# Kernel optimization log

Hardware: AMD Instinct MI355X
Metric: run time of the kernel (lower is better)

The kernel has to match this reference:

```python
import jax, jax.numpy as jnp
import numpy as np

MD = 4            # max_displacement
PATCH = 2 * MD + 1  # 9 displacements per axis (kernel_size=1, stride=1, pad=0)


def setup_inputs() -> dict:
    key = jax.random.key(0)
    k1, k2 = jax.random.split(key)
    feat1 = jax.random.normal(k1, (4, 256, 64, 64), jnp.float32)
    feat2 = jax.random.normal(k2, (4, 256, 64, 64), jnp.float32)
    return {"feat1": feat1, "feat2": feat2}


def _correlation(feat1, feat2, md):
    """SpatialCorrelationSampler with kernel_size=1, patch=2*md+1, stride=1, pad=0.
    out[b,di,dj,y,x] = sum_c feat1[b,c,y,x] * feat2[b,c,y+di-md, x+dj-md] (zero outside).
    Returns (B, P, P, H, W)."""
    B, C, H, W = feat1.shape
    P = 2 * md + 1
    f2p = jnp.pad(feat2, ((0, 0), (0, 0), (md, md), (md, md)))
    # fixed small loop over 81 displacements (not a data-dim loop)
    slices = [
        jnp.sum(feat1 * jax.lax.dynamic_slice(f2p, (0, 0, di, dj), (B, C, H, W)), axis=1)
        for di in range(P) for dj in range(P)
    ]
    return jnp.stack(slices, axis=1).reshape(B, P, P, H, W)


def _remap(cv, md):
    """Vectorized equivalent of remap_cost_volume's python double loop:
    out[b, r+di-md, c+dj-md, r, c] = cv[b, di, dj, r, c] for in-bounds targets."""
    B, P, _, H, W = cv.shape
    d = jnp.arange(P) - md
    r = jnp.arange(H)
    c = jnp.arange(W)
    tr = d[:, None] + r[None, :]            # (P, H) target rows
    tc = d[:, None] + c[None, :]            # (P, W) target cols
    vr = (tr >= 0) & (tr < H)
    vc = (tc >= 0) & (tc < W)
    TR = jnp.clip(tr, 0, H - 1)[:, None, :, None]   # (P,1,H,1)
    TC = jnp.clip(tc, 0, W - 1)[None, :, None, :]   # (1,P,1,W)
    mask = vr[:, None, :, None] & vc[None, :, None, :]  # (P,P,H,W)
    vals = cv * mask.astype(cv.dtype)                   # (B,P,P,H,W)
    R = r[None, None, :, None]
    Cc = c[None, None, None, :]
    TRb, TCb, Rb, Cb = jnp.broadcast_arrays(TR, TC, R, Cc)  # (P,P,H,W)
    out = jnp.zeros((B, H, W, H, W), cv.dtype)
    out = out.at[:, TRb, TCb, Rb, Cb].add(vals)
    return out


def reference(feat1, feat2):
    cv = _correlation(feat1, feat2, MD)      # (B,P,P,H,W)
    B = cv.shape[0]
    H, W = cv.shape[-2], cv.shape[-1]
    remapped = _remap(cv, MD)                # (B,H,W,H,W)
    return remapped.reshape(B, H * W, H, W)  # final .view(B,-1,rows,cols)
```

## Files before the change

### kernel.cpp

```cpp
#include <hip/hip_runtime.h>

#define MD 4
#define PATCH 9
#define NBAND 256
#define NZERO 2048
#define BT 512

__device__ __forceinline__ unsigned bf16b(float x)
{
    unsigned u = __float_as_uint(x);
    return (u + 0x7fffu + ((u >> 16) & 1u)) >> 16;
}

template<int ND>
__device__ __forceinline__ void band_core(
    const float* __restrict__ f1base,
    const unsigned (* __restrict__ sw)[72],
    int ty, int dy0, int lane,
    float acc[3][PATCH])
{
    int yoff[ND];
#pragma unroll
    for (int i = 0; i < ND; ++i) {
        int y = ty + dy0 + i - MD;
        y = y < 0 ? 0 : (y > 63 ? 63 : y);
        yoff[i] = y * 64;
    }

#pragma unroll 2
    for (int cp = 0; cp < 64; ++cp) {
        const float* c0 = f1base + (size_t)(2 * cp) * 4096;
        float f1v0[ND], f1v1[ND];
#pragma unroll
        for (int i = 0; i < ND; ++i) {
            f1v0[i] = c0[yoff[i]];
            f1v1[i] = c0[4096 + yoff[i]];
        }
        const unsigned* wp = &sw[cp][lane];
        unsigned sh2[PATCH];
#pragma unroll
        for (int dxi = 0; dxi < PATCH; ++dxi)
            sh2[dxi] = wp[8 - dxi];
#pragma unroll
        for (int dxi = 0; dxi < PATCH; ++dxi) {
            float lo = __uint_as_float(sh2[dxi] << 16);
            float hi = __uint_as_float(sh2[dxi] & 0xffff0000u);
#pragma unroll
            for (int i = 0; i < ND; ++i) {
                acc[i][dxi] = fmaf(f1v0[i], lo, acc[i][dxi]);
                acc[i][dxi] = fmaf(f1v1[i], hi, acc[i][dxi]);
            }
        }
    }
}

__global__ __launch_bounds__(BT, 8) void cv_kernel(
    const float* __restrict__ f1,
    const float* __restrict__ f2,
    float* __restrict__ out)
{
    const int tid = threadIdx.x;

    if (blockIdx.x >= NBAND) {
        float4* o4 = (float4*)out;
        const float4 z4 = make_float4(0.f, 0.f, 0.f, 0.f);
        const int total4 = 4 * 4096 * 64 * 16;
        const int stride = NZERO * BT;
        for (int i = (blockIdx.x - NBAND) * BT + tid; i < total4; i += stride) {
            int y  = (i >> 4) & 63;
            int ty = (i >> 16) & 63;
            int dy = y - ty;
            if (dy < -MD || dy > MD)
                o4[i] = z4;
        }
        return;
    }

    const int bty = blockIdx.x;
    const int b   = bty >> 6;
    const int ty  = bty & 63;
    const int lane = tid & 63;
    const int w    = tid >> 6;
    const int cq   = w >> 2;
    const int dyg  = w & 3;
    const int dy0  = dyg * 2;
    const int nd   = (dyg == 3) ? 3 : 2;

    __shared__ unsigned uLds[128 * 72];
    unsigned (*sF2)[72] = (unsigned(*)[72])uLds;

    for (int i = tid; i < 128 * 8; i += BT) {
        int c2 = i >> 3, s = i & 7;
        sF2[c2][s < 4 ? s : 64 + s] = 0u;
    }
    const float* f2b = f2 + (size_t)(b * 256) * 4096 + ty * 64;
#pragma unroll
    for (int m = 0; m < 16; ++m) {
        int e  = m * BT + tid;
        int c2 = e >> 6, x = e & 63;
        float lo = f2b[(size_t)(2 * c2) * 4096 + x];
        float hi = f2b[(size_t)(2 * c2 + 1) * 4096 + x];
        sF2[c2][4 + x] = (bf16b(hi) << 16) | bf16b(lo);
    }
    __syncthreads();

    float acc[3][PATCH];
#pragma unroll
    for (int i = 0; i < 3; ++i)
#pragma unroll
        for (int j = 0; j < PATCH; ++j) acc[i][j] = 0.f;

    const float* f1b = f1 + (size_t)(b * 256 + cq * 128) * 4096 + lane;
    const unsigned (*sw)[72] = &sF2[cq * 64];

    if (dyg == 3) band_core<3>(f1b, sw, ty, dy0, lane, acc);
    else          band_core<2>(f1b, sw, ty, dy0, lane, acc);

    __syncthreads();
    float (*sVals)[81] = (float(*)[81])uLds;

    if (cq == 0) {
#pragma unroll
        for (int i = 0; i < 3; ++i) {
            if (i >= nd) continue;
            int dyi = dy0 + i;
            int y = ty + dyi - MD;
            if ((unsigned)y >= 64u) continue;
#pragma unroll
            for (int dxi = 0; dxi < PATCH; ++dxi) {
                int tx = lane - (dxi - MD);
                if ((unsigned)tx < 64u)
                    sVals[tx][dyi * PATCH + dxi] = acc[i][dxi];
            }
        }
    }
    __syncthreads();
    if (cq != 0) {
#pragma unroll
        for (int i = 0; i < 3; ++i) {
            if (i >= nd) continue;
            int dyi = dy0 + i;
            int y = ty + dyi - MD;
            if ((unsigned)y >= 64u) continue;
#pragma unroll
            for (int dxi = 0; dxi < PATCH; ++dxi) {
                int tx = lane - (dxi - MD);
                if ((unsigned)tx < 64u)
                    atomicAdd(&sVals[tx][dyi * PATCH + dxi], acc[i][dxi]);
            }
        }
    }
    __syncthreads();

    float4* out4 = (float4*)(out + (size_t)(b * 4096 + ty * 64) * 4096);
    const int q4 = tid & 15;
    const int ro = tid >> 4;
    for (int rb = 0; rb < 64 * PATCH; rb += 32) {
        int row = rb + ro;
        int tx  = row / PATCH;
        int dyi = row - tx * PATCH;
        int y   = ty + dyi - MD;
        if ((unsigned)y < 64u) {
            float comp[4];
#pragma unroll
            for (int j = 0; j < 4; ++j) {
                int x  = q4 * 4 + j;
                int dx = x - tx;
                comp[j] = (dx >= -MD && dx <= MD) ? sVals[tx][dyi * PATCH + dx + MD] : 0.f;
            }
            out4[tx * 1024 + y * 16 + q4] = make_float4(comp[0], comp[1], comp[2], comp[3]);
        }
    }
}

extern "C" void kernel_launch(void* const* d_in, const int* in_sizes, int n_in,
                              void* d_out, int out_size, void* d_ws, size_t ws_size,
                              hipStream_t stream) {
    const float* f1 = (const float*)d_in[0];
    const float* f2 = (const float*)d_in[1];
    float* out = (float*)d_out;
    cv_kernel<<<NBAND + NZERO, BT, 0, stream>>>(f1, f2, out);
}
```

Baseline: 85.92 us.

## Double block size to split channels four ways and swizzle band block order

Each band block now has 1024 threads. The channel reduction is split into four quarters of 64 channels instead of two halves, and the number of zero-fill blocks is halved. The two-row dy groups use a dual-stream inner loop that processes two channel pairs per iteration for more ILP, and band block indices are swizzled across batches. The intent is more parallelism and latency hiding in the compute phase. In exchange there is more LDS atomic merging, and occupancy is lower per block at the 1024-thread size.

```diff
diff --git a/kernel.cpp b/kernel.cpp
--- a/kernel.cpp
+++ b/kernel.cpp
@@ -3,8 +3,8 @@
 #define MD 4
 #define PATCH 9
 #define NBAND 256
-#define NZERO 2048
-#define BT 512
+#define NZERO 1024
+#define BT 1024
 
 __device__ __forceinline__ unsigned bf16b(float x)
 {
@@ -12,27 +12,76 @@
     return (u + 0x7fffu + ((u >> 16) & 1u)) >> 16;
 }
 
-template<int ND>
-__device__ __forceinline__ void band_core(
+__device__ __forceinline__ void band_core_dual(
     const float* __restrict__ f1base,
     const unsigned (* __restrict__ sw)[72],
     int ty, int dy0, int lane,
     float acc[3][PATCH])
 {
-    int yoff[ND];
-#pragma unroll
-    for (int i = 0; i < ND; ++i) {
+    int yoff[2];
+#pragma unroll
+    for (int i = 0; i < 2; ++i) {
         int y = ty + dy0 + i - MD;
         y = y < 0 ? 0 : (y > 63 ? 63 : y);
         yoff[i] = y * 64;
     }
 
+    for (int cp = 0; cp < 16; ++cp) {
+        const float* cA = f1base + (size_t)(2 * cp) * 4096;
+        const float* cB = cA + (size_t)32 * 4096;
+        float a0[2], a1[2], b0[2], b1[2];
+#pragma unroll
+        for (int i = 0; i < 2; ++i) {
+            a0[i] = cA[yoff[i]];
+            a1[i] = cA[4096 + yoff[i]];
+            b0[i] = cB[yoff[i]];
+            b1[i] = cB[4096 + yoff[i]];
+        }
+        const unsigned* wA = &sw[cp][lane];
+        const unsigned* wB = &sw[cp + 16][lane];
+        unsigned shA[PATCH], shB[PATCH];
+#pragma unroll
+        for (int dxi = 0; dxi < PATCH; ++dxi) {
+            shA[dxi] = wA[8 - dxi];
+            shB[dxi] = wB[8 - dxi];
+        }
+#pragma unroll
+        for (int dxi = 0; dxi < PATCH; ++dxi) {
+            float loA = __uint_as_float(shA[dxi] << 16);
+            float hiA = __uint_as_float(shA[dxi] & 0xffff0000u);
+            float loB = __uint_as_float(shB[dxi] << 16);
+            float hiB = __uint_as_float(shB[dxi] & 0xffff0000u);
+#pragma unroll
+            for (int i = 0; i < 2; ++i) {
+                acc[i][dxi] = fmaf(a0[i], loA, acc[i][dxi]);
+                acc[i][dxi] = fmaf(a1[i], hiA, acc[i][dxi]);
+                acc[i][dxi] = fmaf(b0[i], loB, acc[i][dxi]);
+                acc[i][dxi] = fmaf(b1[i], hiB, acc[i][dxi]);
+            }
+        }
+    }
+}
+
+__device__ __forceinline__ void band_core3(
+    const float* __restrict__ f1base,
+    const unsigned (* __restrict__ sw)[72],
+    int ty, int dy0, int lane,
+    float acc[3][PATCH])
+{
+    int yoff[3];
+#pragma unroll
+    for (int i = 0; i < 3; ++i) {
+        int y = ty + dy0 + i - MD;
+        y = y < 0 ? 0 : (y > 63 ? 63 : y);
+        yoff[i] = y * 64;
+    }
+
 #pragma unroll 2
-    for (int cp = 0; cp < 64; ++cp) {
+    for (int cp = 0; cp < 32; ++cp) {
         const float* c0 = f1base + (size_t)(2 * cp) * 4096;
-        float f1v0[ND], f1v1[ND];
-#pragma unroll
-        for (int i = 0; i < ND; ++i) {
+        float f1v0[3], f1v1[3];
+#pragma unroll
+        for (int i = 0; i < 3; ++i) {
             f1v0[i] = c0[yoff[i]];
             f1v1[i] = c0[4096 + yoff[i]];
         }
@@ -46,7 +95,7 @@
             float lo = __uint_as_float(sh2[dxi] << 16);
             float hi = __uint_as_float(sh2[dxi] & 0xffff0000u);
 #pragma unroll
-            for (int i = 0; i < ND; ++i) {
+            for (int i = 0; i < 3; ++i) {
                 acc[i][dxi] = fmaf(f1v0[i], lo, acc[i][dxi]);
                 acc[i][dxi] = fmaf(f1v1[i], hi, acc[i][dxi]);
             }
@@ -76,7 +125,8 @@
         return;
     }
 
-    const int bty = blockIdx.x;
+    const int bid = blockIdx.x;
+    const int bty = ((bid & 7) << 5) | (bid >> 3);
     const int b   = bty >> 6;
     const int ty  = bty & 63;
     const int lane = tid & 63;
@@ -89,13 +139,13 @@
     __shared__ unsigned uLds[128 * 72];
     unsigned (*sF2)[72] = (unsigned(*)[72])uLds;
 
-    for (int i = tid; i < 128 * 8; i += BT) {
-        int c2 = i >> 3, s = i & 7;
+    {
+        int c2 = tid >> 3, s = tid & 7;
         sF2[c2][s < 4 ? s : 64 + s] = 0u;
     }
     const float* f2b = f2 + (size_t)(b * 256) * 4096 + ty * 64;
 #pragma unroll
-    for (int m = 0; m < 16; ++m) {
+    for (int m = 0; m < 8; ++m) {
         int e  = m * BT + tid;
         int c2 = e >> 6, x = e & 63;
         float lo = f2b[(size_t)(2 * c2) * 4096 + x];
@@ -110,11 +160,11 @@
 #pragma unroll
         for (int j = 0; j < PATCH; ++j) acc[i][j] = 0.f;
 
-    const float* f1b = f1 + (size_t)(b * 256 + cq * 128) * 4096 + lane;
-    const unsigned (*sw)[72] = &sF2[cq * 64];
-
-    if (dyg == 3) band_core<3>(f1b, sw, ty, dy0, lane, acc);
-    else          band_core<2>(f1b, sw, ty, dy0, lane, acc);
+    const float* f1b = f1 + (size_t)(b * 256 + cq * 64) * 4096 + lane;
+    const unsigned (*sw)[72] = &sF2[cq * 32];
+
+    if (dyg == 3) band_core3(f1b, sw, ty, dy0, lane, acc);
+    else          band_core_dual(f1b, sw, ty, dy0, lane, acc);
 
     __syncthreads();
     float (*sVals)[81] = (float(*)[81])uLds;
@@ -155,7 +205,7 @@
     float4* out4 = (float4*)(out + (size_t)(b * 4096 + ty * 64) * 4096);
     const int q4 = tid & 15;
     const int ro = tid >> 4;
-    for (int rb = 0; rb < 64 * PATCH; rb += 32) {
+    for (int rb = 0; rb < 64 * PATCH; rb += 64) {
         int row = rb + ro;
         int tx  = row / PATCH;
         int dyi = row - tx * PATCH;
```

New measurement: 96.86 us. 12.7% more time.
